# Optimization experiments

Measured on AMD Instinct MI355X. Metric: run time of the kernel, lower is better.

## Reference

```python
import jax, jax.numpy as jnp
import numpy as np

EPS = 0.01
EXPD_WEIGHT = 1.0
COMP_WEIGHT = 1.0
NUM_CLASSES = 32
M, D = 262144, 128


def setup_inputs() -> dict:
    key = jax.random.key(0)
    k1, k2 = jax.random.split(key)
    cls_score = jax.random.normal(k1, (M, D), dtype=jnp.float32)
    label = jax.random.randint(k2, (M,), 0, NUM_CLASSES)
    return {"cls_score": cls_score, "label": label}


def _logdet(X):
    sgn, ld = jnp.linalg.slogdet(X)
    return sgn * ld


def reference(cls_score, label):
    m, d = cls_score.shape
    m_f = jnp.asarray(m, cls_score.dtype)
    # expansion term: logdet(c * Z^T Z) / 2, c = d / (m * eps)
    c = d / (m_f * EPS)
    cov = cls_score.T @ cls_score  # [d, d]
    loss_expd = _logdet(c * cov) / 2.0

    # compression term: sum_j m_j/(2m) * logdet(c_j * Z_j^T Z_j)
    def per_class(j):
        mask = (label == j).astype(cls_score.dtype)  # [m]
        m_j = mask.sum()
        safe_mj = jnp.maximum(m_j, 1.0)
        c_j = d / (safe_mj * EPS)
        # Z_j^T Z_j == (mask * Z)^T Z, honoring the boolean subset without gather
        cov_j = (cls_score * mask[:, None]).T @ cls_score  # [d, d]
        ld_j = _logdet(c_j * cov_j)
        return jnp.where(m_j > 0, ld_j * m_j / (2.0 * m_f), 0.0)

    comps = jax.lax.map(per_class, jnp.arange(NUM_CLASSES))  # [J]
    loss_comp = comps.sum()

    # MCR2Loss.forward with return_all=False
    return loss_comp * COMP_WEIGHT - loss_expd * EXPD_WEIGHT
```

## Files before the change

### kernel.cpp

```cpp
#include <hip/hip_runtime.h>
#include <math.h>

#define D 128
#define NCLS 32
#define TSLOT 16
#define CHUNK 256

typedef float f32x16 __attribute__((ext_vector_type(16)));
typedef short bf16x8 __attribute__((ext_vector_type(8)));

__global__ void zero_k(int* hist) {
  int t = threadIdx.x;
  if (t < NCLS) hist[t] = 0;
}

__global__ __launch_bounds__(64) void hist_blk_k(const int* __restrict__ label, int M,
                                                 int NB, int* __restrict__ blkhist_t,
                                                 int* __restrict__ hist) {
  __shared__ int h[NCLS];
  const int lane = threadIdx.x;
  const int b = blockIdx.x;
  if (lane < NCLS) h[lane] = 0;
  __syncthreads();
  const int s0 = b * CHUNK;
#pragma unroll
  for (int it = 0; it < CHUNK / 64; ++it) {
    int i = s0 + it * 64 + lane;
    if (i < M) atomicAdd(&h[label[i]], 1);
  }
  __syncthreads();
  if (lane < NCLS) {
    blkhist_t[lane * NB + b] = h[lane];
    atomicAdd(&hist[lane], h[lane]);
  }
}

__global__ void prefix_k(const int* __restrict__ hist, int* __restrict__ cstart) {
  if (threadIdx.x == 0) {
    int run = 0;
    for (int j = 0; j < NCLS; ++j) { cstart[j] = run; run += hist[j]; }
    cstart[NCLS] = run;
  }
}

__global__ __launch_bounds__(64) void base_k(const int* __restrict__ blkhist_t,
                                             const int* __restrict__ cstart, int NB,
                                             int* __restrict__ base_t) {
  const int j = blockIdx.x;
  const int lane = threadIdx.x;
  const int K = (NB + 63) / 64;
  int vals[32];
  int run = 0;
  for (int k = 0; k < K; ++k) {
    int b = lane * K + k;
    int v = (b < NB) ? blkhist_t[j * NB + b] : 0;
    vals[k] = v;
    run += v;
  }
  int incl = run;
  for (int off = 1; off < 64; off <<= 1) {
    int o = __shfl_up(incl, off);
    if (lane >= off) incl += o;
  }
  int pos = cstart[j] + (incl - run);
  for (int k = 0; k < K; ++k) {
    int b = lane * K + k;
    if (b < NB) base_t[j * NB + b] = pos;
    pos += vals[k];
  }
}

__global__ __launch_bounds__(64) void scatter2_k(const int* __restrict__ label, int M,
                                                 int NB, const int* __restrict__ base_t,
                                                 int* __restrict__ idxbuf) {
  __shared__ int cur[NCLS];
  const int b = blockIdx.x;
  const int lane = threadIdx.x;
  if (lane < NCLS) cur[lane] = base_t[lane * NB + b];
  __syncthreads();
  const int s0 = b * CHUNK;
#pragma unroll
  for (int it = 0; it < CHUNK / 64; ++it) {
    int i = s0 + it * 64 + lane;
    int j = (i < M) ? label[i] : -1;
    unsigned long long mask = 0;
#pragma unroll
    for (int q = 0; q < NCLS; ++q) {
      unsigned long long mm = __ballot(j == q);
      if (j == q) mask = mm;
    }
    if (j >= 0) {
      int myoff = __popcll(mask & ((1ull << lane) - 1ull));
      int basec = cur[j];
      idxbuf[basec + myoff] = i;
      if (myoff == 0) cur[j] = basec + __popcll(mask);
    }
    __syncthreads();
  }
}

__device__ inline void bsplit(float x, short& hi, short& lo) {
  unsigned u = __float_as_uint(x);
  unsigned rh = u + 0x7fffu + ((u >> 16) & 1u);
  unsigned short h = (unsigned short)(rh >> 16);
  float hf = __uint_as_float((unsigned)h << 16);
  float l = x - hf;
  unsigned ul = __float_as_uint(l);
  unsigned rl = ul + 0x7fffu + ((ul >> 16) & 1u);
  hi = (short)h;
  lo = (short)(rl >> 16);
}

__global__ __launch_bounds__(1024, 8) void cov_k(const float* __restrict__ Z,
                                                 const int* __restrict__ idxbuf,
                                                 const int* __restrict__ hist,
                                                 const int* __restrict__ cstart,
                                                 float* __restrict__ partials) {
  __shared__ __attribute__((aligned(16))) char arena[33792];
  char* const ThiB = arena;
  char* const TloB = arena + 16896;

  const int b = blockIdx.x;
  const int cls = b / TSLOT, slot = b % TSLOT;
  const int t = threadIdx.x;
  const int lane = t & 63;
  const int w = t >> 6;
  const int r = w >> 2;
  const int cq = w & 3;

  const int col4 = t & 31;
  const int rg = t >> 5;
  const int wbase = (((rg >> 3) * 4 + (col4 >> 3)) * 2 + ((rg >> 2) & 1)) * 528 +
                    (col4 & 7) * 16 + (rg & 3) * 4;

  const int mj = hist[cls];
  const int seg0 = cstart[cls];
  const int segend = seg0 + mj;
  const int nch = (mj + 63) / 64;

  f32x16 acc;
#pragma unroll
  for (int i = 0; i < 16; ++i) acc[i] = 0.f;

  const int n = lane & 31;
  const int poff = ((n >> 2) + 8 * (n & 3)) * 16 + (lane >> 5) * 528;

  float4 pv[2];
  int idxn0 = 0, idxn1 = 0;
  {
    const int ch = slot;
    const int r0 = seg0 + ch * 64;
    int i0 = 0, i1 = 0;
    if (ch < nch) {
      int g0 = r0 + rg * 2, g1 = r0 + rg * 2 + 1;
      if (g0 < segend) i0 = idxbuf[g0];
      if (g1 < segend) i1 = idxbuf[g1];
      pv[0] = (g0 < segend) ? *(const float4*)(Z + (size_t)i0 * D + col4 * 4)
                            : make_float4(0.f, 0.f, 0.f, 0.f);
      pv[1] = (g1 < segend) ? *(const float4*)(Z + (size_t)i1 * D + col4 * 4)
                            : make_float4(0.f, 0.f, 0.f, 0.f);
    } else {
      pv[0] = make_float4(0.f, 0.f, 0.f, 0.f);
      pv[1] = make_float4(0.f, 0.f, 0.f, 0.f);
    }
    const int chn = ch + TSLOT;
    const int r1 = seg0 + chn * 64;
    if (chn < nch) {
      int g0 = r1 + rg * 2, g1 = r1 + rg * 2 + 1;
      if (g0 < segend) idxn0 = idxbuf[g0];
      if (g1 < segend) idxn1 = idxbuf[g1];
    }
  }

#pragma unroll 1
  for (int ch = slot; ch < nch; ch += TSLOT) {
    __syncthreads();
    {
      float xs[2][4];
      xs[0][0] = pv[0].x; xs[0][1] = pv[0].y; xs[0][2] = pv[0].z; xs[0][3] = pv[0].w;
      xs[1][0] = pv[1].x; xs[1][1] = pv[1].y; xs[1][2] = pv[1].z; xs[1][3] = pv[1].w;
#pragma unroll
      for (int j = 0; j < 4; ++j) {
        short h0, l0, h1, l1;
        bsplit(xs[0][j], h0, l0);
        bsplit(xs[1][j], h1, l1);
        *(short2*)(ThiB + wbase + j * 128) = make_short2(h0, h1);
        *(short2*)(TloB + wbase + j * 128) = make_short2(l0, l1);
      }
    }
    __syncthreads();
    {
      const int chn = ch + TSLOT;
      const int r1 = seg0 + chn * 64;
      int g0 = r1 + rg * 2, g1 = r1 + rg * 2 + 1;
      bool v0 = (chn < nch) && (g0 < segend);
      bool v1 = (chn < nch) && (g1 < segend);
      pv[0] = v0 ? *(const float4*)(Z + (size_t)idxn0 * D + col4 * 4)
                 : make_float4(0.f, 0.f, 0.f, 0.f);
      pv[1] = v1 ? *(const float4*)(Z + (size_t)idxn1 * D + col4 * 4)
                 : make_float4(0.f, 0.f, 0.f, 0.f);
      const int chn2 = ch + 2 * TSLOT;
      const int r2 = seg0 + chn2 * 64;
      if (chn2 < nch) {
        int h0 = r2 + rg * 2, h1 = r2 + rg * 2 + 1;
        if (h0 < segend) idxn0 = idxbuf[h0];
        if (h1 < segend) idxn1 = idxbuf[h1];
      }
    }
#pragma unroll
    for (int kk = 0; kk < 4; ++kk) {
      const int ab = (kk * 4 + r) * 1056 + poff;
      const int bb = (kk * 4 + cq) * 1056 + poff;
      bf16x8 ahi = *(const bf16x8*)(ThiB + ab);
      bf16x8 alo = *(const bf16x8*)(TloB + ab);
      bf16x8 bhi = *(const bf16x8*)(ThiB + bb);
      bf16x8 blo = *(const bf16x8*)(TloB + bb);
      acc = __builtin_amdgcn_mfma_f32_32x32x16_bf16(ahi, bhi, acc, 0, 0, 0);
      acc = __builtin_amdgcn_mfma_f32_32x32x16_bf16(ahi, blo, acc, 0, 0, 0);
      acc = __builtin_amdgcn_mfma_f32_32x32x16_bf16(alo, bhi, acc, 0, 0, 0);
    }
  }

  size_t base = (size_t)b * (D * D);
#pragma unroll
  for (int i = 0; i < 16; ++i) {
    int prow = r * 32 + (i & 3) + 8 * (i >> 2) + 4 * (lane >> 5);
    int qcol = cq * 32 + (lane & 31);
    partials[base + (size_t)prow * D + qcol] = acc[i];
  }
}

__global__ void reduce_k(const float* __restrict__ partials, float* __restrict__ covs) {
  int e = blockIdx.x * blockDim.x + threadIdx.x;
  double tot = 0.0;
  for (int j = 0; j < NCLS; ++j) {
    double s = 0.0;
    for (int t = 0; t < TSLOT; ++t)
      s += (double)partials[(size_t)(j * TSLOT + t) * (D * D) + e];
    covs[(size_t)j * (D * D) + e] = (float)s;
    tot += s;
  }
  covs[(size_t)NCLS * (D * D) + e] = (float)tot;
}

__global__ __launch_bounds__(256, 1) void chol_k(const float* __restrict__ covs,
                                                 const int* __restrict__ hist,
                                                 int Mtot, double* __restrict__ results) {
  __shared__ float As[128][132];
  __shared__ float PlT[32][36];
  __shared__ float invd[32];
  __shared__ float colbuf[32];
  __shared__ double red[64];
  __shared__ __attribute__((aligned(16))) short Thi[96 * 40];
  __shared__ __attribute__((aligned(16))) short Tlo[96 * 40];
  const int j = blockIdx.x;
  const float* A = covs + (size_t)j * (D * D);
  const int tid = threadIdx.x;
  const int lane = tid & 63;
  const int wv = tid >> 6;

#pragma unroll
  for (int it = 0; it < 16; ++it) {
    int e = it * 1024 + tid * 4;
    int r = e >> 7, c = e & 127;
    *(float4*)&As[r][c] = *(const float4*)&A[e];
  }
  __syncthreads();

  double lda = 0.0;
#pragma unroll 1
  for (int p = 0; p < 4; ++p) {
    const int pbase = p * 32;
    const int N2 = 96 - pbase;
    if (wv == 0) {
      const int l = lane & 31;
      float row[32];
#pragma unroll
      for (int c4 = 0; c4 < 8; ++c4) {
        float4 v = *(const float4*)&As[pbase + l][pbase + c4 * 4];
        row[c4 * 4 + 0] = v.x; row[c4 * 4 + 1] = v.y;
        row[c4 * 4 + 2] = v.z; row[c4 * 4 + 3] = v.w;
      }
      float mypiv = 1.f, myinv = 0.f;
#pragma unroll
      for (int k = 0; k < 32; ++k) {
        colbuf[l] = row[k];
        float cb[32];
#pragma unroll
        for (int q = 0; q < 8; ++q) {
          float4 v = *(const float4*)&colbuf[q * 4];
          cb[q * 4 + 0] = v.x; cb[q * 4 + 1] = v.y;
          cb[q * 4 + 2] = v.z; cb[q * 4 + 3] = v.w;
        }
        float piv = cb[k];
        float inv = rsqrtf(piv);
        inv = inv * (1.5f - 0.5f * piv * inv * inv);
        if (lane == k) { mypiv = piv; myinv = inv; }
        float tmul = row[k] * (inv * inv);
#pragma unroll
        for (int c = k + 1; c < 32; ++c)
          row[c] = fmaf(-tmul, cb[c], row[c]);
        row[k] *= inv;
      }
      if (lane < 32) {
#pragma unroll
        for (int c = 0; c < 32; ++c) PlT[c][lane] = row[c];
        invd[lane] = myinv;
      }
      lda += log((double)mypiv);
    }
    __syncthreads();
    if (tid < N2) {
      const int R = pbase + 32 + tid;
      float s[32];
#pragma unroll
      for (int c4 = 0; c4 < 8; ++c4) {
        float4 v = *(const float4*)&As[R][pbase + c4 * 4];
        s[c4 * 4 + 0] = v.x; s[c4 * 4 + 1] = v.y;
        s[c4 * 4 + 2] = v.z; s[c4 * 4 + 3] = v.w;
      }
#pragma unroll
      for (int i = 0; i < 32; ++i) {
        float xi = s[i] * invd[i];
        s[i] = xi;
#pragma unroll
        for (int jj = i + 1; jj < 32; ++jj)
          s[jj] = fmaf(-xi, PlT[i][jj], s[jj]);
      }
      unsigned hp[16], lp[16];
#pragma unroll
      for (int q = 0; q < 16; ++q) {
        short ha, la, hb, lb;
        bsplit(s[2 * q], ha, la);
        bsplit(s[2 * q + 1], hb, lb);
        hp[q] = (unsigned)(unsigned short)ha | ((unsigned)(unsigned short)hb << 16);
        lp[q] = (unsigned)(unsigned short)la | ((unsigned)(unsigned short)lb << 16);
      }
#pragma unroll
      for (int q = 0; q < 4; ++q) {
        *(int4*)&Thi[tid * 40 + q * 8] =
            make_int4(hp[4 * q], hp[4 * q + 1], hp[4 * q + 2], hp[4 * q + 3]);
        *(int4*)&Tlo[tid * 40 + q * 8] =
            make_int4(lp[4 * q], lp[4 * q + 1], lp[4 * q + 2], lp[4 * q + 3]);
      }
    }
    __syncthreads();
    const int nstr = N2 >> 5;
    if (wv < nstr) {
      const int l31 = lane & 31;
      const int h = lane >> 5;
      const int arow = wv * 32 + l31;
#pragma unroll 1
      for (int ct = 0; ct < nstr; ++ct) {
        const int brow = ct * 32 + l31;
        f32x16 acc;
#pragma unroll
        for (int i = 0; i < 16; ++i) acc[i] = 0.f;
#pragma unroll
        for (int ks = 0; ks < 2; ++ks) {
          const int off = ks * 16 + h * 8;
          bf16x8 ahi = *(const bf16x8*)&Thi[arow * 40 + off];
          bf16x8 alo = *(const bf16x8*)&Tlo[arow * 40 + off];
          bf16x8 bhi = *(const bf16x8*)&Thi[brow * 40 + off];
          bf16x8 blo = *(const bf16x8*)&Tlo[brow * 40 + off];
          acc = __builtin_amdgcn_mfma_f32_32x32x16_bf16(ahi, bhi, acc, 0, 0, 0);
          acc = __builtin_amdgcn_mfma_f32_32x32x16_bf16(ahi, blo, acc, 0, 0, 0);
          acc = __builtin_amdgcn_mfma_f32_32x32x16_bf16(alo, bhi, acc, 0, 0, 0);
        }
#pragma unroll
        for (int i = 0; i < 16; ++i) {
          int rr = pbase + 32 + wv * 32 + (i & 3) + 8 * (i >> 2) + 4 * h;
          int cc = pbase + 32 + ct * 32 + l31;
          As[rr][cc] -= acc[i];
        }
      }
    }
    __syncthreads();
  }

  if (wv == 0) red[lane] = lda;
  __syncthreads();
  if (tid == 0) {
    double lsum = 0.0;
    for (int i = 0; i < 64; ++i) lsum += red[i];
    if (j < NCLS) {
      int mj = hist[j];
      double res = 0.0;
      if (mj > 0) {
        double cj = (double)D / ((double)mj * 0.01);
        res = ((double)D * log(cj) + lsum) * (double)mj / (2.0 * (double)Mtot);
      }
      results[j] = res;
    } else {
      double c = (double)D / ((double)Mtot * 0.01);
      results[NCLS] = ((double)D * log(c) + lsum) * 0.5;
    }
  }
}

__global__ void final_k(const double* __restrict__ results, float* __restrict__ out) {
  if (threadIdx.x == 0 && blockIdx.x == 0) {
    double s = 0.0;
    for (int j = 0; j < NCLS; ++j) s += results[j];
    out[0] = (float)(s - results[NCLS]);
  }
}

extern "C" void kernel_launch(void* const* d_in, const int* in_sizes, int n_in,
                              void* d_out, int out_size, void* d_ws, size_t ws_size,
                              hipStream_t stream) {
  const float* Z = (const float*)d_in[0];
  const int* label = (const int*)d_in[1];
  const int Mtot = in_sizes[1];
  float* out = (float*)d_out;
  const int NB = (Mtot + CHUNK - 1) / CHUNK;

  char* ws = (char*)d_ws;
  int* hist = (int*)(ws + 0);
  int* cstart = (int*)(ws + 256);
  double* results = (double*)(ws + 512);
  int* idxbuf = (int*)(ws + 1024);
  float* partials = (float*)(ws + 1024 + (size_t)Mtot * sizeof(int));
  float* covs = partials + (size_t)NCLS * TSLOT * D * D;
  int* blkhist_t = (int*)partials;
  int* base_t = blkhist_t + (size_t)NCLS * NB;

  zero_k<<<1, 64, 0, stream>>>(hist);
  hist_blk_k<<<NB, 64, 0, stream>>>(label, Mtot, NB, blkhist_t, hist);
  prefix_k<<<1, 64, 0, stream>>>(hist, cstart);
  base_k<<<NCLS, 64, 0, stream>>>(blkhist_t, cstart, NB, base_t);
  scatter2_k<<<NB, 64, 0, stream>>>(label, Mtot, NB, base_t, idxbuf);
  cov_k<<<NCLS * TSLOT, 1024, 0, stream>>>(Z, idxbuf, hist, cstart, partials);
  reduce_k<<<(D * D) / 256, 256, 0, stream>>>(partials, covs);
  chol_k<<<NCLS + 1, 256, 0, stream>>>(covs, hist, Mtot, results);
  final_k<<<1, 64, 0, stream>>>(results, out);
}
```

Before: 118.4 us.

## Fuse histogram prefix and final reduction into neighbouring kernels

Drops the zero, prefix and final kernels. Each base block recomputes the per-class totals from the block histograms, block 0 publishes hist and cstart, and the Cholesky kernel uses an atomic last-block counter to do the final sum. This removes three tiny launches and the global atomics. In exchange it adds redundant total computation in every base block and relies on a fence/counter pattern for the final reduction.

```diff
diff --git a/kernel.cpp b/kernel.cpp
--- a/kernel.cpp
+++ b/kernel.cpp
@@ -9,14 +9,8 @@
 typedef float f32x16 __attribute__((ext_vector_type(16)));
 typedef short bf16x8 __attribute__((ext_vector_type(8)));
 
-__global__ void zero_k(int* hist) {
-  int t = threadIdx.x;
-  if (t < NCLS) hist[t] = 0;
-}
-
 __global__ __launch_bounds__(64) void hist_blk_k(const int* __restrict__ label, int M,
-                                                 int NB, int* __restrict__ blkhist_t,
-                                                 int* __restrict__ hist) {
+                                                 int NB, int* __restrict__ blkhist_t) {
   __shared__ int h[NCLS];
   const int lane = threadIdx.x;
   const int b = blockIdx.x;
@@ -29,25 +23,36 @@
     if (i < M) atomicAdd(&h[label[i]], 1);
   }
   __syncthreads();
-  if (lane < NCLS) {
-    blkhist_t[lane * NB + b] = h[lane];
-    atomicAdd(&hist[lane], h[lane]);
-  }
-}
-
-__global__ void prefix_k(const int* __restrict__ hist, int* __restrict__ cstart) {
-  if (threadIdx.x == 0) {
-    int run = 0;
-    for (int j = 0; j < NCLS; ++j) { cstart[j] = run; run += hist[j]; }
-    cstart[NCLS] = run;
-  }
-}
-
-__global__ __launch_bounds__(64) void base_k(const int* __restrict__ blkhist_t,
-                                             const int* __restrict__ cstart, int NB,
-                                             int* __restrict__ base_t) {
+  if (lane < NCLS) blkhist_t[lane * NB + b] = h[lane];
+}
+
+__global__ __launch_bounds__(64) void base2_k(const int* __restrict__ blkhist_t, int NB,
+                                              int* __restrict__ hist,
+                                              int* __restrict__ cstart,
+                                              int* __restrict__ sync_ctr,
+                                              int* __restrict__ base_t) {
   const int j = blockIdx.x;
   const int lane = threadIdx.x;
+  __shared__ int tot[NCLS];
+#pragma unroll 1
+  for (int q = 0; q < NCLS; ++q) {
+    int s = 0;
+    for (int b = lane; b < NB; b += 64) s += blkhist_t[q * NB + b];
+#pragma unroll
+    for (int off = 32; off > 0; off >>= 1) s += __shfl_down(s, off);
+    if (lane == 0) tot[q] = s;
+  }
+  __syncthreads();
+  int mystart = 0;
+  if (lane == 0)
+    for (int q = 0; q < j; ++q) mystart += tot[q];
+  mystart = __shfl(mystart, 0);
+  if (j == 0 && lane == 0) {
+    int run = 0;
+    for (int q = 0; q < NCLS; ++q) { cstart[q] = run; hist[q] = tot[q]; run += tot[q]; }
+    cstart[NCLS] = run;
+    *sync_ctr = 0;
+  }
   const int K = (NB + 63) / 64;
   int vals[32];
   int run = 0;
@@ -62,7 +67,7 @@
     int o = __shfl_up(incl, off);
     if (lane >= off) incl += o;
   }
-  int pos = cstart[j] + (incl - run);
+  int pos = mystart + (incl - run);
   for (int k = 0; k < K; ++k) {
     int b = lane * K + k;
     if (b < NB) base_t[j * NB + b] = pos;
@@ -245,7 +250,9 @@
 
 __global__ __launch_bounds__(256, 1) void chol_k(const float* __restrict__ covs,
                                                  const int* __restrict__ hist,
-                                                 int Mtot, double* __restrict__ results) {
+                                                 int Mtot, double* __restrict__ results,
+                                                 int* __restrict__ sync_ctr,
+                                                 float* __restrict__ out) {
   __shared__ float As[128][132];
   __shared__ float PlT[32][36];
   __shared__ float invd[32];
@@ -383,26 +390,28 @@
   if (tid == 0) {
     double lsum = 0.0;
     for (int i = 0; i < 64; ++i) lsum += red[i];
+    double res;
     if (j < NCLS) {
       int mj = hist[j];
-      double res = 0.0;
+      res = 0.0;
       if (mj > 0) {
         double cj = (double)D / ((double)mj * 0.01);
         res = ((double)D * log(cj) + lsum) * (double)mj / (2.0 * (double)Mtot);
       }
-      results[j] = res;
     } else {
       double c = (double)D / ((double)Mtot * 0.01);
-      results[NCLS] = ((double)D * log(c) + lsum) * 0.5;
-    }
-  }
-}
-
-__global__ void final_k(const double* __restrict__ results, float* __restrict__ out) {
-  if (threadIdx.x == 0 && blockIdx.x == 0) {
-    double s = 0.0;
-    for (int j = 0; j < NCLS; ++j) s += results[j];
-    out[0] = (float)(s - results[NCLS]);
+      res = ((double)D * log(c) + lsum) * 0.5;
+    }
+    results[j] = res;
+    __threadfence();
+    int done = atomicAdd(sync_ctr, 1);
+    if (done == NCLS) {
+      __threadfence();
+      volatile double* vr = (volatile double*)results;
+      double ssum = 0.0;
+      for (int q = 0; q < NCLS; ++q) ssum += vr[q];
+      out[0] = (float)(ssum - vr[NCLS]);
+    }
   }
 }
 
@@ -418,6 +427,7 @@
   char* ws = (char*)d_ws;
   int* hist = (int*)(ws + 0);
   int* cstart = (int*)(ws + 256);
+  int* sync_ctr = (int*)(ws + 448);
   double* results = (double*)(ws + 512);
   int* idxbuf = (int*)(ws + 1024);
   float* partials = (float*)(ws + 1024 + (size_t)Mtot * sizeof(int));
@@ -425,13 +435,10 @@
   int* blkhist_t = (int*)partials;
   int* base_t = blkhist_t + (size_t)NCLS * NB;
 
-  zero_k<<<1, 64, 0, stream>>>(hist);
-  hist_blk_k<<<NB, 64, 0, stream>>>(label, Mtot, NB, blkhist_t, hist);
-  prefix_k<<<1, 64, 0, stream>>>(hist, cstart);
-  base_k<<<NCLS, 64, 0, stream>>>(blkhist_t, cstart, NB, base_t);
+  hist_blk_k<<<NB, 64, 0, stream>>>(label, Mtot, NB, blkhist_t);
+  base2_k<<<NCLS, 64, 0, stream>>>(blkhist_t, NB, hist, cstart, sync_ctr, base_t);
   scatter2_k<<<NB, 64, 0, stream>>>(label, Mtot, NB, base_t, idxbuf);
   cov_k<<<NCLS * TSLOT, 1024, 0, stream>>>(Z, idxbuf, hist, cstart, partials);
   reduce_k<<<(D * D) / 256, 256, 0, stream>>>(partials, covs);
-  chol_k<<<NCLS + 1, 256, 0, stream>>>(covs, hist, Mtot, results);
-  final_k<<<1, 64, 0, stream>>>(results, out);
-}
+  chol_k<<<NCLS + 1, 256, 0, stream>>>(covs, hist, Mtot, results, sync_ctr, out);
+}
```

After: 183.3 us. 1.55x slower.

## Double-buffer gathered rows two chunks ahead and use raw LDS barriers

Applied to the files above, without the earlier changes.

The covariance loop is unrolled by two, with separate register buffers A and B. Global gathers now run two chunks ahead, which hides more latency on the indexed Z row loads. __syncthreads is replaced by a custom barrier that waits only on LDS counters and not on outstanding global loads, so prefetches stay in flight across barriers. This costs more registers under launch_bounds(1024,8). Odd chunk counts also do an extra zero-filled MFMA pass.

```diff
diff --git a/kernel.cpp b/kernel.cpp
--- a/kernel.cpp
+++ b/kernel.cpp
@@ -111,6 +111,12 @@
   lo = (short)(rl >> 16);
 }
 
+__device__ __forceinline__ void rawbar() {
+  asm volatile("s_waitcnt lgkmcnt(0)" ::: "memory");
+  __builtin_amdgcn_s_barrier();
+  __builtin_amdgcn_sched_barrier(0);
+}
+
 __global__ __launch_bounds__(1024, 8) void cov_k(const float* __restrict__ Z,
                                                  const int* __restrict__ idxbuf,
                                                  const int* __restrict__ hist,
@@ -145,40 +151,64 @@
   const int n = lane & 31;
   const int poff = ((n >> 2) + 8 * (n & 3)) * 16 + (lane >> 5) * 528;
 
-  float4 pv[2];
-  int idxn0 = 0, idxn1 = 0;
+  float4 pvA[2], pvB[2];
+  int iA0 = 0, iA1 = 0;
+  int iB0 = 0, iB1 = 0;
+
   {
-    const int ch = slot;
-    const int r0 = seg0 + ch * 64;
+    const int c0 = slot;
+    const int r0 = seg0 + c0 * 64;
     int i0 = 0, i1 = 0;
-    if (ch < nch) {
-      int g0 = r0 + rg * 2, g1 = r0 + rg * 2 + 1;
+    if (c0 < nch) {
+      int g0 = r0 + rg * 2, g1 = g0 + 1;
       if (g0 < segend) i0 = idxbuf[g0];
       if (g1 < segend) i1 = idxbuf[g1];
-      pv[0] = (g0 < segend) ? *(const float4*)(Z + (size_t)i0 * D + col4 * 4)
-                            : make_float4(0.f, 0.f, 0.f, 0.f);
-      pv[1] = (g1 < segend) ? *(const float4*)(Z + (size_t)i1 * D + col4 * 4)
-                            : make_float4(0.f, 0.f, 0.f, 0.f);
+      pvA[0] = (g0 < segend) ? *(const float4*)(Z + (size_t)i0 * D + col4 * 4)
+                             : make_float4(0.f, 0.f, 0.f, 0.f);
+      pvA[1] = (g1 < segend) ? *(const float4*)(Z + (size_t)i1 * D + col4 * 4)
+                             : make_float4(0.f, 0.f, 0.f, 0.f);
     } else {
-      pv[0] = make_float4(0.f, 0.f, 0.f, 0.f);
-      pv[1] = make_float4(0.f, 0.f, 0.f, 0.f);
-    }
-    const int chn = ch + TSLOT;
-    const int r1 = seg0 + chn * 64;
-    if (chn < nch) {
-      int g0 = r1 + rg * 2, g1 = r1 + rg * 2 + 1;
-      if (g0 < segend) idxn0 = idxbuf[g0];
-      if (g1 < segend) idxn1 = idxbuf[g1];
+      pvA[0] = make_float4(0.f, 0.f, 0.f, 0.f);
+      pvA[1] = make_float4(0.f, 0.f, 0.f, 0.f);
+    }
+    const int c1 = slot + TSLOT;
+    const int r1 = seg0 + c1 * 64;
+    int j0 = 0, j1 = 0;
+    if (c1 < nch) {
+      int g0 = r1 + rg * 2, g1 = g0 + 1;
+      if (g0 < segend) j0 = idxbuf[g0];
+      if (g1 < segend) j1 = idxbuf[g1];
+      pvB[0] = (g0 < segend) ? *(const float4*)(Z + (size_t)j0 * D + col4 * 4)
+                             : make_float4(0.f, 0.f, 0.f, 0.f);
+      pvB[1] = (g1 < segend) ? *(const float4*)(Z + (size_t)j1 * D + col4 * 4)
+                             : make_float4(0.f, 0.f, 0.f, 0.f);
+    } else {
+      pvB[0] = make_float4(0.f, 0.f, 0.f, 0.f);
+      pvB[1] = make_float4(0.f, 0.f, 0.f, 0.f);
+    }
+    const int c2 = slot + 2 * TSLOT;
+    const int r2 = seg0 + c2 * 64;
+    if (c2 < nch) {
+      int g0 = r2 + rg * 2, g1 = g0 + 1;
+      if (g0 < segend) iA0 = idxbuf[g0];
+      if (g1 < segend) iA1 = idxbuf[g1];
+    }
+    const int c3 = slot + 3 * TSLOT;
+    const int r3 = seg0 + c3 * 64;
+    if (c3 < nch) {
+      int g0 = r3 + rg * 2, g1 = g0 + 1;
+      if (g0 < segend) iB0 = idxbuf[g0];
+      if (g1 < segend) iB1 = idxbuf[g1];
     }
   }
 
 #pragma unroll 1
-  for (int ch = slot; ch < nch; ch += TSLOT) {
-    __syncthreads();
+  for (int ch = slot; ch < nch; ch += 2 * TSLOT) {
+    rawbar();
     {
       float xs[2][4];
-      xs[0][0] = pv[0].x; xs[0][1] = pv[0].y; xs[0][2] = pv[0].z; xs[0][3] = pv[0].w;
-      xs[1][0] = pv[1].x; xs[1][1] = pv[1].y; xs[1][2] = pv[1].z; xs[1][3] = pv[1].w;
+      xs[0][0] = pvA[0].x; xs[0][1] = pvA[0].y; xs[0][2] = pvA[0].z; xs[0][3] = pvA[0].w;
+      xs[1][0] = pvA[1].x; xs[1][1] = pvA[1].y; xs[1][2] = pvA[1].z; xs[1][3] = pvA[1].w;
 #pragma unroll
       for (int j = 0; j < 4; ++j) {
         short h0, l0, h1, l1;
@@ -188,23 +218,68 @@
         *(short2*)(TloB + wbase + j * 128) = make_short2(l0, l1);
       }
     }
-    __syncthreads();
+    rawbar();
     {
-      const int chn = ch + TSLOT;
-      const int r1 = seg0 + chn * 64;
-      int g0 = r1 + rg * 2, g1 = r1 + rg * 2 + 1;
+      const int chn = ch + 2 * TSLOT;
+      const int rn = seg0 + chn * 64;
+      int g0 = rn + rg * 2, g1 = g0 + 1;
       bool v0 = (chn < nch) && (g0 < segend);
       bool v1 = (chn < nch) && (g1 < segend);
-      pv[0] = v0 ? *(const float4*)(Z + (size_t)idxn0 * D + col4 * 4)
-                 : make_float4(0.f, 0.f, 0.f, 0.f);
-      pv[1] = v1 ? *(const float4*)(Z + (size_t)idxn1 * D + col4 * 4)
-                 : make_float4(0.f, 0.f, 0.f, 0.f);
-      const int chn2 = ch + 2 * TSLOT;
-      const int r2 = seg0 + chn2 * 64;
-      if (chn2 < nch) {
-        int h0 = r2 + rg * 2, h1 = r2 + rg * 2 + 1;
-        if (h0 < segend) idxn0 = idxbuf[h0];
-        if (h1 < segend) idxn1 = idxbuf[h1];
+      pvA[0] = v0 ? *(const float4*)(Z + (size_t)iA0 * D + col4 * 4)
+                  : make_float4(0.f, 0.f, 0.f, 0.f);
+      pvA[1] = v1 ? *(const float4*)(Z + (size_t)iA1 * D + col4 * 4)
+                  : make_float4(0.f, 0.f, 0.f, 0.f);
+      const int c4 = ch + 4 * TSLOT;
+      const int r4 = seg0 + c4 * 64;
+      if (c4 < nch) {
+        int h0 = r4 + rg * 2, h1 = h0 + 1;
+        if (h0 < segend) iA0 = idxbuf[h0];
+        if (h1 < segend) iA1 = idxbuf[h1];
+      }
+    }
+#pragma unroll
+    for (int kk = 0; kk < 4; ++kk) {
+      const int ab = (kk * 4 + r) * 1056 + poff;
+      const int bb = (kk * 4 + cq) * 1056 + poff;
+      bf16x8 ahi = *(const bf16x8*)(ThiB + ab);
+      bf16x8 alo = *(const bf16x8*)(TloB + ab);
+      bf16x8 bhi = *(const bf16x8*)(ThiB + bb);
+      bf16x8 blo = *(const bf16x8*)(TloB + bb);
+      acc = __builtin_amdgcn_mfma_f32_32x32x16_bf16(ahi, bhi, acc, 0, 0, 0);
+      acc = __builtin_amdgcn_mfma_f32_32x32x16_bf16(ahi, blo, acc, 0, 0, 0);
+      acc = __builtin_amdgcn_mfma_f32_32x32x16_bf16(alo, bhi, acc, 0, 0, 0);
+    }
+    rawbar();
+    {
+      float xs[2][4];
+      xs[0][0] = pvB[0].x; xs[0][1] = pvB[0].y; xs[0][2] = pvB[0].z; xs[0][3] = pvB[0].w;
+      xs[1][0] = pvB[1].x; xs[1][1] = pvB[1].y; xs[1][2] = pvB[1].z; xs[1][3] = pvB[1].w;
+#pragma unroll
+      for (int j = 0; j < 4; ++j) {
+        short h0, l0, h1, l1;
+        bsplit(xs[0][j], h0, l0);
+        bsplit(xs[1][j], h1, l1);
+        *(short2*)(ThiB + wbase + j * 128) = make_short2(h0, h1);
+        *(short2*)(TloB + wbase + j * 128) = make_short2(l0, l1);
+      }
+    }
+    rawbar();
+    {
+      const int chn = ch + 3 * TSLOT;
+      const int rn = seg0 + chn * 64;
+      int g0 = rn + rg * 2, g1 = g0 + 1;
+      bool v0 = (chn < nch) && (g0 < segend);
+      bool v1 = (chn < nch) && (g1 < segend);
+      pvB[0] = v0 ? *(const float4*)(Z + (size_t)iB0 * D + col4 * 4)
+                  : make_float4(0.f, 0.f, 0.f, 0.f);
+      pvB[1] = v1 ? *(const float4*)(Z + (size_t)iB1 * D + col4 * 4)
+                  : make_float4(0.f, 0.f, 0.f, 0.f);
+      const int c5 = ch + 5 * TSLOT;
+      const int r5 = seg0 + c5 * 64;
+      if (c5 < nch) {
+        int h0 = r5 + rg * 2, h1 = h0 + 1;
+        if (h0 < segend) iB0 = idxbuf[h0];
+        if (h1 < segend) iB1 = idxbuf[h1];
       }
     }
 #pragma unroll
```

Result: slower. 123.0 us (+3.9%).
